# Performance work log

Measured on AMD Instinct MI355X. Metric: run time of the kernel, lower is better.

## Reference

```python
import jax, jax.numpy as jnp
import numpy as np
from jax import lax

NUM_SKETCH = 3
BN_EPS = 1e-5


def setup_inputs() -> dict:
    key = jax.random.key(0)
    ks = jax.random.split(key, 8)
    B, C, H, W = 32, 128, 64, 64
    D = C // 4  # comp_rate = 4
    k = 3
    x = jax.random.normal(ks[0], (B, C, H, W), dtype=jnp.float32)
    fan = C * k * k
    w1 = jax.random.normal(ks[1], (C, C, k, k), dtype=jnp.float32) / np.sqrt(fan)
    w2 = jax.random.normal(ks[2], (C, C, k, k), dtype=jnp.float32) / np.sqrt(fan)
    gamma1 = jnp.ones((C,), jnp.float32); beta1 = jnp.zeros((C,), jnp.float32)
    gamma2 = jnp.ones((C,), jnp.float32); beta2 = jnp.zeros((C,), jnp.float32)
    # count-sketch hash matrices: hs[j] is (D, C), each column c has a single 1
    idx = jax.random.randint(ks[3], (NUM_SKETCH, C), 0, D)
    hs = jax.nn.one_hot(idx, D, dtype=jnp.float32).transpose(0, 2, 1)  # (3, D, C)
    ss = (jax.random.randint(ks[4], (NUM_SKETCH, C), 0, 2) * 2 - 1).astype(jnp.float32)  # (3, C) signs
    return {"x": x, "w1": w1, "w2": w2, "gamma1": gamma1, "beta1": beta1,
            "gamma2": gamma2, "beta2": beta2, "hs": hs, "ss": ss}


def _sketch_conv_unsketch(x, w, hs, ss):
    # w: (Co, Ci, k, k); hs: (J, D, Co); ss: (J, Co)
    Co, Ci, k, _ = w.shape
    J, D, _ = hs.shape
    B, _, H, W = x.shape
    wf = w.reshape(Co, -1)  # (Co, M)
    # sketched weights per sketch j: h_j @ (wf * s_j[:, None])
    w_sk = jnp.einsum('jdc,jc,cm->jdm', hs, ss, wf).reshape(J * D, Ci, k, k)
    # one conv with J*D output channels (padding=1, stride=1 hardcoded in source)
    y = lax.conv_general_dilated(x, w_sk, window_strides=(1, 1),
                                 padding=[(1, 1), (1, 1)],
                                 dimension_numbers=('NCHW', 'OIHW', 'NCHW'))
    y = y.reshape(B, J, D, H, W)
    # unsketch activations: h_j^T @ y_j, then sign scale (num_s=1 so inner median is identity)
    y_un = jnp.einsum('jdc,bjdhw->jbchw', hs, y) * ss[:, None, :, None, None]
    return jnp.median(y_un, axis=0)  # median over the 3 sketches -> (B, Co, H, W)


def _bn_relu(y, gamma, beta):
    # BatchNorm2d in training mode: biased batch stats over (N, H, W)
    mean = jnp.mean(y, axis=(0, 2, 3), keepdims=True)
    var = jnp.var(y, axis=(0, 2, 3), keepdims=True)
    yhat = (y - mean) * lax.rsqrt(var + BN_EPS)
    return jax.nn.relu(yhat * gamma[None, :, None, None] + beta[None, :, None, None])


def reference(x, w1, w2, gamma1, beta1, gamma2, beta2, hs, ss):
    residual = x
    out1 = _bn_relu(_sketch_conv_unsketch(x, w1, hs, ss), gamma1, beta1)
    del out1  # faithful to source bug: second conv loop uses x, discarding out1
    out = _bn_relu(_sketch_conv_unsketch(x, w2, hs, ss), gamma2, beta2)
    return out + residual
```

## Files before the change

kernel.cpp:

```cpp
#include <hip/hip_runtime.h>
#include <stdint.h>

typedef __bf16 bf16x8 __attribute__((ext_vector_type(8)));
typedef float  f32x4  __attribute__((ext_vector_type(4)));

static constexpr int Bn = 32, Cn = 128, Hn = 64, Wn = 64, HWn = 4096;
static constexpr size_t OFF_XT    = 0;
static constexpr size_t OFF_WF    = 33554432;
static constexpr size_t OFF_IDX   = 33775616;
static constexpr size_t OFF_M     = 33777152;
static constexpr size_t OFF_STATS = 67331584;
static constexpr size_t OFF_BN    = 67332608;

__device__ __forceinline__ unsigned short f32_to_bf16(float f) {
    union { float f; unsigned u; } v; v.f = f;
    unsigned u = v.u;
    return (unsigned short)((u + 0x7FFFu + ((u >> 16) & 1u)) >> 16);
}
__device__ __forceinline__ float bf16_to_f32(unsigned short h) {
    union { unsigned u; float f; } v; v.u = ((unsigned)h) << 16;
    return v.f;
}

__global__ __launch_bounds__(256) void k_transpose(const float* __restrict__ x,
                                                   unsigned short* __restrict__ xT) {
    __shared__ __align__(16) unsigned short sm[256 * 40];
    int blk = blockIdx.x;
    int pt = blk & 15, q = (blk >> 4) & 3, b = blk >> 6;
    int p0 = pt * 256;
    int t = threadIdx.x;
    const float* xp = x + ((size_t)(b * Cn + q * 32) * HWn) + p0 + t;
#pragma unroll
    for (int cil = 0; cil < 32; ++cil)
        sm[t * 40 + cil] = f32_to_bf16(xp[(size_t)cil * HWn]);
    __syncthreads();
    uint4* dst = (uint4*)(xT + ((size_t)(b * 4 + q) * HWn + p0) * 32);
#pragma unroll
    for (int pass = 0; pass < 4; ++pass) {
        int pix = pass * 64 + (t >> 2);
        int ch  = t & 3;
        dst[pix * 4 + ch] = *(const uint4*)(&sm[pix * 40 + ch * 8]);
    }
}

__global__ void k_idx(const float* __restrict__ hs, int* __restrict__ idx) {
    int t = blockIdx.x * 256 + threadIdx.x;
    if (t >= 384) return;
    int j = t >> 7, c = t & 127;
    int found = 0;
    for (int d = 0; d < 32; ++d)
        if (hs[(j * 32 + d) * 128 + c] > 0.5f) found = d;
    idx[t] = found;
}

__global__ __launch_bounds__(256) void k_wsk(const float* __restrict__ w2,
                                             const float* __restrict__ hs,
                                             const float* __restrict__ ss,
                                             unsigned short* __restrict__ wf) {
    int f = blockIdx.x * 256 + threadIdx.x;
    int jj   = f & 7;
    int lane = (f >> 3) & 63;
    int nt   = (f >> 9) % 6;
    int qt   = f / (512 * 6);
    int t    = qt % 9;
    int q    = qt / 9;
    int k  = ((lane >> 4) << 3) + jj;
    int ci = q * 32 + k;
    int n  = nt * 16 + (lane & 15);
    int j = n >> 5, d = n & 31;
    float sum = 0.f;
    for (int c = 0; c < 128; ++c) {
        float g = hs[(j * 32 + d) * 128 + c];
        if (g != 0.f) sum += g * ss[j * 128 + c] * w2[(c * 128 + ci) * 9 + t];
    }
    wf[f] = f32_to_bf16(sum);
}

__global__ __launch_bounds__(256, 2) void k_conv(const unsigned short* __restrict__ xT,
                                                 const unsigned short* __restrict__ wf,
                                                 const int* __restrict__ idx,
                                                 const float* __restrict__ ss,
                                                 unsigned short* __restrict__ m_out) {
    __shared__ __align__(16) unsigned short sm[25088];
    __shared__ int   idx_sh[384];
    __shared__ float ss_sh[384];
    int tid  = threadIdx.x;
    int blk  = blockIdx.x;
    int tile = blk & 15, b = blk >> 4;
    int ty0  = tile * 4;
    int wv   = tid >> 6, lane = tid & 63;
    int quad = lane >> 4, l15 = lane & 15;

    for (int i = tid; i < 384; i += 256) { idx_sh[i] = idx[i]; ss_sh[i] = ss[i]; }

    f32x4 acc[4][6];
#pragma unroll
    for (int a = 0; a < 4; ++a)
#pragma unroll
        for (int nb = 0; nb < 6; ++nb) acc[a][nb] = (f32x4){0.f, 0.f, 0.f, 0.f};

    const unsigned short* wl = wf + lane * 8;

    for (int q = 0; q < 4; ++q) {
        __syncthreads();
#pragma unroll
        for (int pass = 0; pass < 2; ++pass) {
            int r = tid + pass * 256;
            if (r < 396) {
                int hy = r / 66, hx = r - hy * 66;
                int gy = ty0 + hy - 1, gx = hx - 1;
                uint4* dst = (uint4*)(&sm[r * 40]);
                if (gy >= 0 && gy < 64 && gx >= 0 && gx < 64) {
                    const uint4* src = (const uint4*)(xT + ((size_t)(b * 4 + q) * HWn + gy * 64 + gx) * 32);
                    dst[0] = src[0]; dst[1] = src[1]; dst[2] = src[2]; dst[3] = src[3];
                } else {
                    uint4 z = {0u, 0u, 0u, 0u};
                    dst[0] = z; dst[1] = z; dst[2] = z; dst[3] = z;
                }
            }
        }
        __syncthreads();
#pragma unroll
        for (int tp = 0; tp < 9; ++tp) {
            int dy = tp / 3, dx = tp % 3;
            bf16x8 afr[4];
#pragma unroll
            for (int mq = 0; mq < 4; ++mq) {
                int off = ((wv + dy) * 66 + mq * 16 + l15 + dx) * 40 + quad * 8;
                afr[mq] = *(const bf16x8*)(&sm[off]);
            }
            bf16x8 bfr[6];
            const unsigned short* wb = wl + (size_t)((q * 9 + tp) * 6) * 512;
#pragma unroll
            for (int nb = 0; nb < 6; ++nb)
                bfr[nb] = *(const bf16x8*)(wb + nb * 512);
#pragma unroll
            for (int mq = 0; mq < 4; ++mq)
#pragma unroll
                for (int nb = 0; nb < 6; ++nb)
                    acc[mq][nb] = __builtin_amdgcn_mfma_f32_16x16x32_bf16(afr[mq], bfr[nb], acc[mq][nb], 0, 0, 0);
        }
    }
    __syncthreads();
#pragma unroll
    for (int mq = 0; mq < 4; ++mq) {
#pragma unroll
        for (int nb = 0; nb < 6; ++nb) {
            int ch = nb * 16 + l15;
            int pbase = wv * 64 + mq * 16 + quad * 4;
#pragma unroll
            for (int r = 0; r < 4; ++r)
                sm[(pbase + r) * 98 + ch] = f32_to_bf16(acc[mq][nb][r]);
        }
    }
    __syncthreads();
    int p = tid;
    unsigned short* mp = m_out + (size_t)b * Cn * HWn + tile * 256 + tid;
#pragma unroll 4
    for (int c = 0; c < 128; ++c) {
        int i0 = idx_sh[c], i1 = idx_sh[128 + c], i2 = idx_sh[256 + c];
        float z0 = ss_sh[c]       * bf16_to_f32(sm[p * 98 + i0]);
        float z1 = ss_sh[128 + c] * bf16_to_f32(sm[p * 98 + 32 + i1]);
        float z2 = ss_sh[256 + c] * bf16_to_f32(sm[p * 98 + 64 + i2]);
        float lo = fminf(z0, z1), hi = fmaxf(z0, z1);
        float med = fmaxf(lo, fminf(hi, z2));
        mp[(size_t)c * HWn] = f32_to_bf16(med);
    }
}

__global__ __launch_bounds__(256) void k_stats(const unsigned short* __restrict__ m,
                                               float* __restrict__ stats) {
    int blk = blockIdx.x;
    int c = blk >> 2, bq = blk & 3;
    int tid = threadIdx.x;
    float s = 0.f, s2 = 0.f;
    for (int b = bq * 8; b < bq * 8 + 8; ++b) {
        const ushort4* mp = (const ushort4*)(m + (size_t)(b * Cn + c) * HWn);
#pragma unroll
        for (int i = 0; i < 4; ++i) {
            ushort4 v = mp[i * 256 + tid];
            float a0 = bf16_to_f32(v.x), a1 = bf16_to_f32(v.y);
            float a2 = bf16_to_f32(v.z), a3 = bf16_to_f32(v.w);
            s  += a0 + a1 + a2 + a3;
            s2 += a0 * a0 + a1 * a1 + a2 * a2 + a3 * a3;
        }
    }
    for (int o = 32; o > 0; o >>= 1) { s += __shfl_down(s, o); s2 += __shfl_down(s2, o); }
    __shared__ float rs[8];
    if ((tid & 63) == 0) { rs[tid >> 6] = s; rs[4 + (tid >> 6)] = s2; }
    __syncthreads();
    if (tid == 0) {
        float S = rs[0] + rs[1] + rs[2] + rs[3];
        float S2 = rs[4] + rs[5] + rs[6] + rs[7];
        atomicAdd(&stats[c], S);
        atomicAdd(&stats[128 + c], S2);
    }
}

__global__ void k_bn(const float* __restrict__ stats, const float* __restrict__ gamma,
                     const float* __restrict__ beta, float* __restrict__ bn) {
    int c = threadIdx.x;
    if (c < 128) {
        const float N = 131072.f;
        float mean = stats[c] / N;
        float var  = stats[128 + c] / N - mean * mean;
        float sc   = gamma[c] * rsqrtf(var + 1e-5f);
        bn[c] = sc;
        bn[128 + c] = beta[c] - mean * sc;
    }
}

__global__ __launch_bounds__(256) void k_apply(const unsigned short* __restrict__ m,
                                               const float* __restrict__ x,
                                               const float* __restrict__ bn,
                                               float* __restrict__ out) {
    int i4 = blockIdx.x * 256 + threadIdx.x;
    size_t base = (size_t)i4 * 4;
    int c = (int)((base >> 12) & 127);
    float sc = bn[c], sh = bn[128 + c];
    ushort4 mv = ((const ushort4*)m)[i4];
    float4  xv = ((const float4*)x)[i4];
    float4 o;
    o.x = fmaxf(bf16_to_f32(mv.x) * sc + sh, 0.f) + xv.x;
    o.y = fmaxf(bf16_to_f32(mv.y) * sc + sh, 0.f) + xv.y;
    o.z = fmaxf(bf16_to_f32(mv.z) * sc + sh, 0.f) + xv.z;
    o.w = fmaxf(bf16_to_f32(mv.w) * sc + sh, 0.f) + xv.w;
    ((float4*)out)[i4] = o;
}

extern "C" void kernel_launch(void* const* d_in, const int* in_sizes, int n_in,
                              void* d_out, int out_size, void* d_ws, size_t ws_size,
                              hipStream_t stream) {
    const float* x      = (const float*)d_in[0];
    const float* w2     = (const float*)d_in[2];
    const float* gamma2 = (const float*)d_in[5];
    const float* beta2  = (const float*)d_in[6];
    const float* hs     = (const float*)d_in[7];
    const float* ss     = (const float*)d_in[8];
    float* out = (float*)d_out;

    char* ws = (char*)d_ws;
    unsigned short* xT  = (unsigned short*)(ws + OFF_XT);
    unsigned short* wfp = (unsigned short*)(ws + OFF_WF);
    int*            idp = (int*)(ws + OFF_IDX);
    unsigned short* mp  = (unsigned short*)(ws + OFF_M);
    float*          st  = (float*)(ws + OFF_STATS);
    float*          bnp = (float*)(ws + OFF_BN);

    hipMemsetAsync(st, 0, 1024, stream);
    k_transpose<<<2048, 256, 0, stream>>>(x, xT);
    k_idx<<<2, 256, 0, stream>>>(hs, idp);
    k_wsk<<<432, 256, 0, stream>>>(w2, hs, ss, wfp);
    k_conv<<<512, 256, 0, stream>>>(xT, wfp, idp, ss, mp);
    k_stats<<<512, 256, 0, stream>>>(mp, st);
    k_bn<<<1, 128, 0, stream>>>(st, gamma2, beta2, bnp);
    k_apply<<<16384, 256, 0, stream>>>(mp, x, bnp, out);
}
```

Measured before the change: 225.3 us.

## Fuse BN stats into conv, halve conv tile, prefetch next input slab in registers

The conv kernel now computes per-channel sum and sum-of-squares of the median output itself, using wave shuffles and shared partials followed by atomics. This removes the separate stats kernel and its re-read of the intermediate tensor. Tiles shrink to 2 rows with 1024 blocks, each wave covering half the output channels, which cuts shared memory and allows 4 blocks per CU. The next channel-quarter input is prefetched into registers while MFMAs run on the current one. The cost is one shuffle reduction per channel in the epilogue and a smaller MFMA tile per wave, so each weight fragment is reused less.

```diff
diff --git a/kernel.cpp b/kernel.cpp
--- a/kernel.cpp
+++ b/kernel.cpp
@@ -76,88 +76,117 @@
     wf[f] = f32_to_bf16(sum);
 }
 
-__global__ __launch_bounds__(256, 2) void k_conv(const unsigned short* __restrict__ xT,
+__global__ __launch_bounds__(256, 4) void k_conv(const unsigned short* __restrict__ xT,
                                                  const unsigned short* __restrict__ wf,
                                                  const int* __restrict__ idx,
                                                  const float* __restrict__ ss,
-                                                 unsigned short* __restrict__ m_out) {
-    __shared__ __align__(16) unsigned short sm[25088];
+                                                 unsigned short* __restrict__ m_out,
+                                                 float* __restrict__ stats) {
+    __shared__ __align__(16) unsigned short sm[12544];
     __shared__ int   idx_sh[384];
     __shared__ float ss_sh[384];
+    __shared__ float part_s[256];
+    __shared__ float part_s2[256];
     int tid  = threadIdx.x;
     int blk  = blockIdx.x;
-    int tile = blk & 15, b = blk >> 4;
-    int ty0  = tile * 4;
+    int tile = blk & 31, b = blk >> 5;
+    int ty0  = tile * 2;
     int wv   = tid >> 6, lane = tid & 63;
     int quad = lane >> 4, l15 = lane & 15;
+    int row_l = wv >> 1, nh = wv & 1;
 
     for (int i = tid; i < 384; i += 256) { idx_sh[i] = idx[i]; ss_sh[i] = ss[i]; }
 
-    f32x4 acc[4][6];
+    int goff[5], loff[5];
+#pragma unroll
+    for (int i = 0; i < 5; ++i) {
+        int k = (i < 4) ? (tid + i * 256) : (1024 + tid);
+        bool act = (i < 4) || (tid < 32);
+        int r = k >> 2, ch = k & 3;
+        int hy = r / 66, hx = r - hy * 66;
+        int gy = ty0 + hy - 1, gx = hx - 1;
+        bool inb = act && gy >= 0 && gy < 64 && gx >= 0 && gx < 64;
+        goff[i] = inb ? ((gy * 64 + gx) * 32 + ch * 8) : -1;
+        loff[i] = r * 40 + ch * 8;
+    }
+
+    f32x4 acc[4][3];
 #pragma unroll
     for (int a = 0; a < 4; ++a)
 #pragma unroll
-        for (int nb = 0; nb < 6; ++nb) acc[a][nb] = (f32x4){0.f, 0.f, 0.f, 0.f};
-
-    const unsigned short* wl = wf + lane * 8;
+        for (int nb = 0; nb < 3; ++nb) acc[a][nb] = (f32x4){0.f, 0.f, 0.f, 0.f};
+
+    const uint4 z4 = {0u, 0u, 0u, 0u};
+    uint4 h[5];
+
+    {
+        const unsigned short* xq = xT + (size_t)(b * 4) * (HWn * 32);
+#pragma unroll
+        for (int i = 0; i < 4; ++i)
+            h[i] = (goff[i] >= 0) ? *(const uint4*)(xq + goff[i]) : z4;
+        if (tid < 32) h[4] = (goff[4] >= 0) ? *(const uint4*)(xq + goff[4]) : z4;
+#pragma unroll
+        for (int i = 0; i < 4; ++i) *(uint4*)(&sm[loff[i]]) = h[i];
+        if (tid < 32) *(uint4*)(&sm[loff[4]]) = h[4];
+    }
+    __syncthreads();
+
+    const unsigned short* wl = wf + (size_t)(nh * 3) * 512 + lane * 8;
 
     for (int q = 0; q < 4; ++q) {
-        __syncthreads();
-#pragma unroll
-        for (int pass = 0; pass < 2; ++pass) {
-            int r = tid + pass * 256;
-            if (r < 396) {
-                int hy = r / 66, hx = r - hy * 66;
-                int gy = ty0 + hy - 1, gx = hx - 1;
-                uint4* dst = (uint4*)(&sm[r * 40]);
-                if (gy >= 0 && gy < 64 && gx >= 0 && gx < 64) {
-                    const uint4* src = (const uint4*)(xT + ((size_t)(b * 4 + q) * HWn + gy * 64 + gx) * 32);
-                    dst[0] = src[0]; dst[1] = src[1]; dst[2] = src[2]; dst[3] = src[3];
-                } else {
-                    uint4 z = {0u, 0u, 0u, 0u};
-                    dst[0] = z; dst[1] = z; dst[2] = z; dst[3] = z;
-                }
-            }
-        }
-        __syncthreads();
+        if (q < 3) {
+            const unsigned short* xq = xT + (size_t)(b * 4 + q + 1) * (HWn * 32);
+#pragma unroll
+            for (int i = 0; i < 4; ++i)
+                h[i] = (goff[i] >= 0) ? *(const uint4*)(xq + goff[i]) : z4;
+            if (tid < 32) h[4] = (goff[4] >= 0) ? *(const uint4*)(xq + goff[4]) : z4;
+        }
+        const unsigned short* wq = wl + (size_t)(q * 9 * 6) * 512;
 #pragma unroll
         for (int tp = 0; tp < 9; ++tp) {
             int dy = tp / 3, dx = tp % 3;
             bf16x8 afr[4];
 #pragma unroll
             for (int mq = 0; mq < 4; ++mq) {
-                int off = ((wv + dy) * 66 + mq * 16 + l15 + dx) * 40 + quad * 8;
+                int off = ((row_l + dy) * 66 + mq * 16 + l15 + dx) * 40 + quad * 8;
                 afr[mq] = *(const bf16x8*)(&sm[off]);
             }
-            bf16x8 bfr[6];
-            const unsigned short* wb = wl + (size_t)((q * 9 + tp) * 6) * 512;
-#pragma unroll
-            for (int nb = 0; nb < 6; ++nb)
+            bf16x8 bfr[3];
+            const unsigned short* wb = wq + (size_t)(tp * 6) * 512;
+#pragma unroll
+            for (int nb = 0; nb < 3; ++nb)
                 bfr[nb] = *(const bf16x8*)(wb + nb * 512);
 #pragma unroll
             for (int mq = 0; mq < 4; ++mq)
 #pragma unroll
-                for (int nb = 0; nb < 6; ++nb)
+                for (int nb = 0; nb < 3; ++nb)
                     acc[mq][nb] = __builtin_amdgcn_mfma_f32_16x16x32_bf16(afr[mq], bfr[nb], acc[mq][nb], 0, 0, 0);
         }
-    }
-    __syncthreads();
+        __syncthreads();
+        if (q < 3) {
+#pragma unroll
+            for (int i = 0; i < 4; ++i) *(uint4*)(&sm[loff[i]]) = h[i];
+            if (tid < 32) *(uint4*)(&sm[loff[4]]) = h[4];
+            __syncthreads();
+        }
+    }
 #pragma unroll
     for (int mq = 0; mq < 4; ++mq) {
 #pragma unroll
-        for (int nb = 0; nb < 6; ++nb) {
-            int ch = nb * 16 + l15;
-            int pbase = wv * 64 + mq * 16 + quad * 4;
+        for (int nb = 0; nb < 3; ++nb) {
+            int ch = (nh * 3 + nb) * 16 + l15;
+            int pbase = row_l * 64 + mq * 16 + quad * 4;
 #pragma unroll
             for (int r = 0; r < 4; ++r)
                 sm[(pbase + r) * 98 + ch] = f32_to_bf16(acc[mq][nb][r]);
         }
     }
     __syncthreads();
-    int p = tid;
-    unsigned short* mp = m_out + (size_t)b * Cn * HWn + tile * 256 + tid;
-#pragma unroll 4
-    for (int c = 0; c < 128; ++c) {
+    int p = tid & 127, c0 = (tid >> 7) * 64;
+    unsigned short* mp = m_out + (size_t)b * Cn * HWn + tile * 128 + p;
+#pragma unroll 2
+    for (int cc = 0; cc < 64; ++cc) {
+        int c = c0 + cc;
         int i0 = idx_sh[c], i1 = idx_sh[128 + c], i2 = idx_sh[256 + c];
         float z0 = ss_sh[c]       * bf16_to_f32(sm[p * 98 + i0]);
         float z1 = ss_sh[128 + c] * bf16_to_f32(sm[p * 98 + 32 + i1]);
@@ -165,33 +194,16 @@
         float lo = fminf(z0, z1), hi = fmaxf(z0, z1);
         float med = fmaxf(lo, fminf(hi, z2));
         mp[(size_t)c * HWn] = f32_to_bf16(med);
-    }
-}
-
-__global__ __launch_bounds__(256) void k_stats(const unsigned short* __restrict__ m,
-                                               float* __restrict__ stats) {
-    int blk = blockIdx.x;
-    int c = blk >> 2, bq = blk & 3;
-    int tid = threadIdx.x;
-    float s = 0.f, s2 = 0.f;
-    for (int b = bq * 8; b < bq * 8 + 8; ++b) {
-        const ushort4* mp = (const ushort4*)(m + (size_t)(b * Cn + c) * HWn);
-#pragma unroll
-        for (int i = 0; i < 4; ++i) {
-            ushort4 v = mp[i * 256 + tid];
-            float a0 = bf16_to_f32(v.x), a1 = bf16_to_f32(v.y);
-            float a2 = bf16_to_f32(v.z), a3 = bf16_to_f32(v.w);
-            s  += a0 + a1 + a2 + a3;
-            s2 += a0 * a0 + a1 * a1 + a2 * a2 + a3 * a3;
-        }
-    }
-    for (int o = 32; o > 0; o >>= 1) { s += __shfl_down(s, o); s2 += __shfl_down(s2, o); }
-    __shared__ float rs[8];
-    if ((tid & 63) == 0) { rs[tid >> 6] = s; rs[4 + (tid >> 6)] = s2; }
-    __syncthreads();
-    if (tid == 0) {
-        float S = rs[0] + rs[1] + rs[2] + rs[3];
-        float S2 = rs[4] + rs[5] + rs[6] + rs[7];
+        float s = med, s2 = med * med;
+#pragma unroll
+        for (int o = 32; o > 0; o >>= 1) { s += __shfl_xor(s, o); s2 += __shfl_xor(s2, o); }
+        if (lane == 0) { part_s[wv * 64 + cc] = s; part_s2[wv * 64 + cc] = s2; }
+    }
+    __syncthreads();
+    if (tid < 128) {
+        int c = tid, g = (c >> 6) * 2, cl = c & 63;
+        float S  = part_s[g * 64 + cl]  + part_s[(g + 1) * 64 + cl];
+        float S2 = part_s2[g * 64 + cl] + part_s2[(g + 1) * 64 + cl];
         atomicAdd(&stats[c], S);
         atomicAdd(&stats[128 + c], S2);
     }
@@ -251,8 +263,7 @@
     k_transpose<<<2048, 256, 0, stream>>>(x, xT);
     k_idx<<<2, 256, 0, stream>>>(hs, idp);
     k_wsk<<<432, 256, 0, stream>>>(w2, hs, ss, wfp);
-    k_conv<<<512, 256, 0, stream>>>(xT, wfp, idp, ss, mp);
-    k_stats<<<512, 256, 0, stream>>>(mp, st);
+    k_conv<<<1024, 256, 0, stream>>>(xT, wfp, idp, ss, mp, st);
     k_bn<<<1, 128, 0, stream>>>(st, gamma2, beta2, bnp);
     k_apply<<<16384, 256, 0, stream>>>(mp, x, bnp, out);
 }
```

Result: slower. 271.6 us (+20.5%).

## Fuse BN statistics into conv epilogue and prefetch next input tile

Applied to the files above, without the earlier changes.

Removes the separate stats kernel by computing per-channel sum and sum of squares inside the conv epilogue, reduced with wave shuffles and then atomics. The epilogue is reorganised into a channel-major shared-memory layout so median and store use vectorised 16-byte accesses. The main loop now prefetches the next input-channel slab into registers and double-buffers the weight fragments so loads overlap the MFMA work. The costs are more registers and many more atomics, one per channel per half-wave in every block.

```diff
diff --git a/kernel.cpp b/kernel.cpp
--- a/kernel.cpp
+++ b/kernel.cpp
@@ -20,6 +20,16 @@
 __device__ __forceinline__ float bf16_to_f32(unsigned short h) {
     union { unsigned u; float f; } v; v.u = ((unsigned)h) << 16;
     return v.f;
+}
+__device__ __forceinline__ float bf_lo(unsigned w) {
+    union { unsigned u; float f; } v; v.u = w << 16; return v.f;
+}
+__device__ __forceinline__ float bf_hi(unsigned w) {
+    union { unsigned u; float f; } v; v.u = w & 0xffff0000u; return v.f;
+}
+__device__ __forceinline__ float med3(float z0, float z1, float z2) {
+    float lo = fminf(z0, z1), hi = fmaxf(z0, z1);
+    return fmaxf(lo, fminf(hi, z2));
 }
 
 __global__ __launch_bounds__(256) void k_transpose(const float* __restrict__ x,
@@ -80,8 +90,9 @@
                                                  const unsigned short* __restrict__ wf,
                                                  const int* __restrict__ idx,
                                                  const float* __restrict__ ss,
-                                                 unsigned short* __restrict__ m_out) {
-    __shared__ __align__(16) unsigned short sm[25088];
+                                                 unsigned short* __restrict__ m_out,
+                                                 float* __restrict__ stats) {
+    __shared__ __align__(16) unsigned short sm[25344];
     __shared__ int   idx_sh[384];
     __shared__ float ss_sh[384];
     int tid  = threadIdx.x;
@@ -93,35 +104,62 @@
 
     for (int i = tid; i < 384; i += 256) { idx_sh[i] = idx[i]; ss_sh[i] = ss[i]; }
 
+    int goff[7], loff[7];
+#pragma unroll
+    for (int i = 0; i < 7; ++i) {
+        int k = tid + i * 256;
+        if (k < 1584) {
+            int r = k >> 2, ch = k & 3;
+            int hy = r / 66, hx = r - hy * 66;
+            int gy = ty0 + hy - 1, gx = hx - 1;
+            loff[i] = r * 40 + ch * 8;
+            goff[i] = (gy >= 0 && gy < 64 && gx >= 0 && gx < 64)
+                    ? ((gy * 64 + gx) * 32 + ch * 8) : -1;
+        } else { loff[i] = -1; goff[i] = -1; }
+    }
+
     f32x4 acc[4][6];
 #pragma unroll
     for (int a = 0; a < 4; ++a)
 #pragma unroll
         for (int nb = 0; nb < 6; ++nb) acc[a][nb] = (f32x4){0.f, 0.f, 0.f, 0.f};
 
+    const uint4 z4 = {0u, 0u, 0u, 0u};
+    uint4 h[7];
+
+    {
+        const unsigned short* xq = xT + (size_t)(b * 4) * (HWn * 32);
+#pragma unroll
+        for (int i = 0; i < 7; ++i)
+            if (loff[i] >= 0) {
+                uint4 v = (goff[i] >= 0) ? *(const uint4*)(xq + goff[i]) : z4;
+                *(uint4*)(&sm[loff[i]]) = v;
+            }
+    }
+    __syncthreads();
+
     const unsigned short* wl = wf + lane * 8;
 
     for (int q = 0; q < 4; ++q) {
-        __syncthreads();
-#pragma unroll
-        for (int pass = 0; pass < 2; ++pass) {
-            int r = tid + pass * 256;
-            if (r < 396) {
-                int hy = r / 66, hx = r - hy * 66;
-                int gy = ty0 + hy - 1, gx = hx - 1;
-                uint4* dst = (uint4*)(&sm[r * 40]);
-                if (gy >= 0 && gy < 64 && gx >= 0 && gx < 64) {
-                    const uint4* src = (const uint4*)(xT + ((size_t)(b * 4 + q) * HWn + gy * 64 + gx) * 32);
-                    dst[0] = src[0]; dst[1] = src[1]; dst[2] = src[2]; dst[3] = src[3];
-                } else {
-                    uint4 z = {0u, 0u, 0u, 0u};
-                    dst[0] = z; dst[1] = z; dst[2] = z; dst[3] = z;
-                }
+        if (q < 3) {
+            const unsigned short* xq = xT + (size_t)(b * 4 + q + 1) * (HWn * 32);
+#pragma unroll
+            for (int i = 0; i < 7; ++i)
+                h[i] = (loff[i] >= 0 && goff[i] >= 0) ? *(const uint4*)(xq + goff[i]) : z4;
+        }
+        const unsigned short* wq = wl + (size_t)(q * 54) * 512;
+        bf16x8 bfr[2][6];
+#pragma unroll
+        for (int nb = 0; nb < 6; ++nb) bfr[0][nb] = *(const bf16x8*)(wq + nb * 512);
+#pragma unroll
+        for (int tp = 0; tp < 9; ++tp) {
+            int cur = tp & 1;
+            if (tp < 8) {
+                const unsigned short* wb = wq + (size_t)((tp + 1) * 6) * 512;
+#pragma unroll
+                for (int nb = 0; nb < 6; ++nb)
+                    bfr[cur ^ 1][nb] = *(const bf16x8*)(wb + nb * 512);
             }
-        }
-        __syncthreads();
-#pragma unroll
-        for (int tp = 0; tp < 9; ++tp) {
             int dy = tp / 3, dx = tp % 3;
             bf16x8 afr[4];
 #pragma unroll
@@ -129,71 +167,64 @@
                 int off = ((wv + dy) * 66 + mq * 16 + l15 + dx) * 40 + quad * 8;
                 afr[mq] = *(const bf16x8*)(&sm[off]);
             }
-            bf16x8 bfr[6];
-            const unsigned short* wb = wl + (size_t)((q * 9 + tp) * 6) * 512;
-#pragma unroll
-            for (int nb = 0; nb < 6; ++nb)
-                bfr[nb] = *(const bf16x8*)(wb + nb * 512);
 #pragma unroll
             for (int mq = 0; mq < 4; ++mq)
 #pragma unroll
                 for (int nb = 0; nb < 6; ++nb)
-                    acc[mq][nb] = __builtin_amdgcn_mfma_f32_16x16x32_bf16(afr[mq], bfr[nb], acc[mq][nb], 0, 0, 0);
-        }
-    }
-    __syncthreads();
-#pragma unroll
-    for (int mq = 0; mq < 4; ++mq) {
+                    acc[mq][nb] = __builtin_amdgcn_mfma_f32_16x16x32_bf16(afr[mq], bfr[cur][nb], acc[mq][nb], 0, 0, 0);
+        }
+        __syncthreads();
+        if (q < 3) {
+#pragma unroll
+            for (int i = 0; i < 7; ++i)
+                if (loff[i] >= 0) *(uint4*)(&sm[loff[i]]) = h[i];
+            __syncthreads();
+        }
+    }
+
+#pragma unroll
+    for (int mq = 0; mq < 4; ++mq)
 #pragma unroll
         for (int nb = 0; nb < 6; ++nb) {
             int ch = nb * 16 + l15;
-            int pbase = wv * 64 + mq * 16 + quad * 4;
-#pragma unroll
-            for (int r = 0; r < 4; ++r)
-                sm[(pbase + r) * 98 + ch] = f32_to_bf16(acc[mq][nb][r]);
-        }
-    }
+            int px = wv * 64 + mq * 16 + quad * 4;
+            ushort4 v;
+            v.x = f32_to_bf16(acc[mq][nb][0]);
+            v.y = f32_to_bf16(acc[mq][nb][1]);
+            v.z = f32_to_bf16(acc[mq][nb][2]);
+            v.w = f32_to_bf16(acc[mq][nb][3]);
+            *(ushort4*)(&sm[ch * 264 + px]) = v;
+        }
     __syncthreads();
-    int p = tid;
-    unsigned short* mp = m_out + (size_t)b * Cn * HWn + tile * 256 + tid;
-#pragma unroll 4
-    for (int c = 0; c < 128; ++c) {
-        int i0 = idx_sh[c], i1 = idx_sh[128 + c], i2 = idx_sh[256 + c];
-        float z0 = ss_sh[c]       * bf16_to_f32(sm[p * 98 + i0]);
-        float z1 = ss_sh[128 + c] * bf16_to_f32(sm[p * 98 + 32 + i1]);
-        float z2 = ss_sh[256 + c] * bf16_to_f32(sm[p * 98 + 64 + i2]);
-        float lo = fminf(z0, z1), hi = fmaxf(z0, z1);
-        float med = fmaxf(lo, fminf(hi, z2));
-        mp[(size_t)c * HWn] = f32_to_bf16(med);
-    }
-}
-
-__global__ __launch_bounds__(256) void k_stats(const unsigned short* __restrict__ m,
-                                               float* __restrict__ stats) {
-    int blk = blockIdx.x;
-    int c = blk >> 2, bq = blk & 3;
-    int tid = threadIdx.x;
-    float s = 0.f, s2 = 0.f;
-    for (int b = bq * 8; b < bq * 8 + 8; ++b) {
-        const ushort4* mp = (const ushort4*)(m + (size_t)(b * Cn + c) * HWn);
-#pragma unroll
-        for (int i = 0; i < 4; ++i) {
-            ushort4 v = mp[i * 256 + tid];
-            float a0 = bf16_to_f32(v.x), a1 = bf16_to_f32(v.y);
-            float a2 = bf16_to_f32(v.z), a3 = bf16_to_f32(v.w);
-            s  += a0 + a1 + a2 + a3;
-            s2 += a0 * a0 + a1 * a1 + a2 * a2 + a3 * a3;
-        }
-    }
-    for (int o = 32; o > 0; o >>= 1) { s += __shfl_down(s, o); s2 += __shfl_down(s2, o); }
-    __shared__ float rs[8];
-    if ((tid & 63) == 0) { rs[tid >> 6] = s; rs[4 + (tid >> 6)] = s2; }
-    __syncthreads();
-    if (tid == 0) {
-        float S = rs[0] + rs[1] + rs[2] + rs[3];
-        float S2 = rs[4] + rs[5] + rs[6] + rs[7];
-        atomicAdd(&stats[c], S);
-        atomicAdd(&stats[128 + c], S2);
+
+    int half = lane >> 5, p8 = lane & 31;
+    unsigned short* mpb = m_out + (size_t)b * Cn * HWn + tile * 256 + p8 * 8;
+#pragma unroll 2
+    for (int i = 0; i < 16; ++i) {
+        int c = wv * 32 + i * 2 + half;
+        int r0 = idx_sh[c], r1 = 32 + idx_sh[128 + c], r2 = 64 + idx_sh[256 + c];
+        float sg0 = ss_sh[c], sg1 = ss_sh[128 + c], sg2 = ss_sh[256 + c];
+        uint4 w0 = *(const uint4*)(&sm[r0 * 264 + p8 * 8]);
+        uint4 w1 = *(const uint4*)(&sm[r1 * 264 + p8 * 8]);
+        uint4 w2v = *(const uint4*)(&sm[r2 * 264 + p8 * 8]);
+        const unsigned* u0 = (const unsigned*)&w0;
+        const unsigned* u1 = (const unsigned*)&w1;
+        const unsigned* u2 = (const unsigned*)&w2v;
+        uint4 R;
+        unsigned* rw = (unsigned*)&R;
+        float s = 0.f, s2 = 0.f;
+#pragma unroll
+        for (int e = 0; e < 4; ++e) {
+            float mlo = med3(sg0 * bf_lo(u0[e]), sg1 * bf_lo(u1[e]), sg2 * bf_lo(u2[e]));
+            float mhi = med3(sg0 * bf_hi(u0[e]), sg1 * bf_hi(u1[e]), sg2 * bf_hi(u2[e]));
+            s  += mlo + mhi;
+            s2 += mlo * mlo + mhi * mhi;
+            rw[e] = (unsigned)f32_to_bf16(mlo) | ((unsigned)f32_to_bf16(mhi) << 16);
+        }
+        *(uint4*)(mpb + (size_t)c * HWn) = R;
+#pragma unroll
+        for (int o = 16; o > 0; o >>= 1) { s += __shfl_xor(s, o); s2 += __shfl_xor(s2, o); }
+        if ((lane & 31) == 0) { atomicAdd(&stats[c], s); atomicAdd(&stats[128 + c], s2); }
     }
 }
 
@@ -251,8 +282,7 @@
     k_transpose<<<2048, 256, 0, stream>>>(x, xT);
     k_idx<<<2, 256, 0, stream>>>(hs, idp);
     k_wsk<<<432, 256, 0, stream>>>(w2, hs, ss, wfp);
-    k_conv<<<512, 256, 0, stream>>>(xT, wfp, idp, ss, mp);
-    k_stats<<<512, 256, 0, stream>>>(mp, st);
+    k_conv<<<512, 256, 0, stream>>>(xT, wfp, idp, ss, mp, st);
     k_bn<<<1, 128, 0, stream>>>(st, gamma2, beta2, bnp);
     k_apply<<<16384, 256, 0, stream>>>(mp, x, bnp, out);
 }
```

Measured after the change: 318.8 us. 1.42x slower.
